# Kernel tuning notes

Measured on AMD Instinct MI355X. Metric: run time of the kernel, lower is better.

The kernel has to match this reference:

```python
import jax, jax.numpy as jnp
import numpy as np

N = 100000
E = 1600000
IN_CH = 128
HID = 16
HEADS = 4
OUT_CH = 2
EDGE_DIM = 3
NEG_SLOPE = 0.2


def gat_layer(x, src, dst, e_feat, W, att_src, att_dst, We, att_edge, bias, H, C, concat):
    # x: [N, Fin] -> projected [N, H, C]
    xs = (x @ W).reshape(-1, H, C)
    a_src = jnp.sum(xs * att_src, axis=-1)          # [N, H]
    a_dst = jnp.sum(xs * att_dst, axis=-1)          # [N, H]
    ee = (e_feat @ We).reshape(-1, H, C)            # [E, H, C]
    a_edge = jnp.sum(ee * att_edge, axis=-1)        # [E, H]
    alpha = a_src[src] + a_dst[dst] + a_edge        # [E, H]
    alpha = jax.nn.leaky_relu(alpha, NEG_SLOPE)
    # segment softmax over incoming edges of each dst node
    seg_max = jax.ops.segment_max(alpha, dst, num_segments=N)
    alpha = jnp.exp(alpha - seg_max[dst])
    seg_sum = jax.ops.segment_sum(alpha, dst, num_segments=N)
    alpha = alpha / (seg_sum[dst] + 1e-16)
    # weighted message aggregation
    msg = xs[src] * alpha[:, :, None]               # [E, H, C]
    out = jax.ops.segment_sum(msg, dst, num_segments=N)  # [N, H, C]
    out = out.reshape(-1, H * C) if concat else out.mean(axis=1)
    return out + bias


def setup_inputs() -> dict:
    key = jax.random.key(0)
    ks = jax.random.split(key, 24)
    g = lambda i, shape, scale=0.1: jax.random.normal(ks[i], shape, dtype=jnp.float32) * scale
    inp = {
        "x": jax.random.normal(ks[0], (N, IN_CH), dtype=jnp.float32),
        "edge_index": jax.random.randint(ks[1], (2, E), 0, N, dtype=jnp.int32),
        "edge_feat": jax.random.normal(ks[2], (E, EDGE_DIM), dtype=jnp.float32),
        # edge MLP
        "Em1": g(3, (EDGE_DIM, EDGE_DIM)), "eb1": g(4, (EDGE_DIM,)),
        "Em2": g(5, (EDGE_DIM, EDGE_DIM)), "eb2": g(6, (EDGE_DIM,)),
        # conv1: in -> HID per head, HEADS heads, concat
        "W1": g(7, (IN_CH, HEADS * HID)),
        "as1": g(8, (HEADS, HID)), "ad1": g(9, (HEADS, HID)),
        "We1": g(10, (EDGE_DIM, HEADS * HID)), "ae1": g(11, (HEADS, HID)),
        "b1": g(12, (HEADS * HID,)),
        # conv2: HEADS*HID -> OUT_CH, 1 head, no concat
        "W2": g(13, (HEADS * HID, OUT_CH)),
        "as2": g(14, (1, OUT_CH)), "ad2": g(15, (1, OUT_CH)),
        "We2": g(16, (EDGE_DIM, OUT_CH)), "ae2": g(17, (1, OUT_CH)),
        "b2": g(18, (OUT_CH,)),
    }
    return inp


def reference(x, edge_index, edge_feat,
              Em1, eb1, Em2, eb2,
              W1, as1, ad1, We1, ae1, b1,
              W2, as2, ad2, We2, ae2, b2):
    src, dst = edge_index[0], edge_index[1]
    # edge MLP: Linear -> ReLU -> Linear
    e = jax.nn.relu(edge_feat @ Em1 + eb1) @ Em2 + eb2
    # dropout layers are identity in eval mode
    h = gat_layer(x, src, dst, e, W1, as1, ad1, We1, ae1, b1, HEADS, HID, concat=True)
    h = jax.nn.elu(h)
    out = gat_layer(h, src, dst, e, W2, as2, ad2, We2, ae2, b2, 1, OUT_CH, concat=False)
    return out
```

## Files before the change

### kernel.cpp

```cpp
#include <hip/hip_runtime.h>
#include <hip/hip_fp16.h>
#include <math.h>
#include <stdint.h>

#define NEG_SLOPE 0.2f
#define SCAN_TILE 2048

__device__ __forceinline__ float leaky(float a) { return a > 0.f ? a : NEG_SLOPE * a; }
__device__ __forceinline__ __half2 u2h2(unsigned u) { return *reinterpret_cast<__half2*>(&u); }

__global__ __launch_bounds__(256) void k_pw(const int* __restrict__ dst, int* __restrict__ deg8,
                                            int* __restrict__ pw, int E, int N,
                                            const float* __restrict__ We1, const float* __restrict__ ae1,
                                            const float* __restrict__ We2, const float* __restrict__ ae2,
                                            float* __restrict__ cw) {
    if (blockIdx.x == 0 && threadIdx.x == 0) {
        for (int i = 0; i < 3; i++)
            for (int h = 0; h < 4; h++) {
                float s = 0.f;
                for (int m = 0; m < 16; m++) s += We1[i*64 + h*16 + m] * ae1[h*16 + m];
                cw[i*4 + h] = s;
            }
        for (int i = 0; i < 3; i++) cw[12 + i] = We2[i*2]*ae2[0] + We2[i*2+1]*ae2[1];
    }
    int c = blockIdx.x & 7;
    int* deg = deg8 + (size_t)c * N;
    unsigned ctag = (unsigned)c << 28;
    int base = (blockIdx.x * blockDim.x + threadIdx.x) * 4;
    if (base >= E) return;
    if (base + 3 < E) {
        int4 dv = *reinterpret_cast<const int4*>(&dst[base]);
        int4 pv;
        pv.x = atomicAdd(&deg[dv.x], 1) | ctag;
        pv.y = atomicAdd(&deg[dv.y], 1) | ctag;
        pv.z = atomicAdd(&deg[dv.z], 1) | ctag;
        pv.w = atomicAdd(&deg[dv.w], 1) | ctag;
        *reinterpret_cast<int4*>(&pw[base]) = pv;
    } else {
        for (int i = base; i < E; i++) pw[i] = atomicAdd(&deg[dst[i]], 1) | ctag;
    }
}

__global__ __launch_bounds__(256) void k_scan_partial(const int* __restrict__ deg8, int* __restrict__ tsum, int N) {
    __shared__ int sh[256];
    int b = blockIdx.x, t = threadIdx.x;
    int base = b * SCAN_TILE + t * 8;
    int s = 0;
    if (base + 8 <= N) {
        for (int c = 0; c < 8; c++) {
            const int4* p4 = reinterpret_cast<const int4*>(deg8 + (size_t)c * N + base);
            int4 a = p4[0], bb = p4[1];
            s += a.x + a.y + a.z + a.w + bb.x + bb.y + bb.z + bb.w;
        }
    } else if (base < N) {
        for (int i = base; i < N; i++)
            for (int c = 0; c < 8; c++) s += deg8[(size_t)c * N + i];
    }
    sh[t] = s; __syncthreads();
    for (int o = 128; o > 0; o >>= 1) { if (t < o) sh[t] += sh[t + o]; __syncthreads(); }
    if (t == 0) tsum[b] = sh[0];
}

__global__ void k_scan_tsum(const int* __restrict__ tsum, int* __restrict__ toff,
                            int* __restrict__ rowptr, int nb, int N) {
    if (threadIdx.x == 0 && blockIdx.x == 0) {
        int run = 0;
        for (int i = 0; i < nb; i++) { toff[i] = run; run += tsum[i]; }
        rowptr[N] = run;
    }
}

__global__ __launch_bounds__(256) void k_scan_final(const int* __restrict__ deg8, const int* __restrict__ toff,
        int* __restrict__ rowptr, int* __restrict__ cmbi, int N) {
    __shared__ int sh[256];
    int b = blockIdx.x, t = threadIdx.x;
    int base = b * SCAN_TILE + t * 8;
    int vt[8]; int s = 0;
    #pragma unroll
    for (int i = 0; i < 8; i++) {
        int idx = base + i; int tot = 0;
        if (idx < N) {
            #pragma unroll
            for (int c = 0; c < 8; c++) tot += deg8[(size_t)c * N + idx];
        }
        vt[i] = tot; s += tot;
    }
    sh[t] = s; __syncthreads();
    for (int o = 1; o < 256; o <<= 1) {
        int u = (t >= o) ? sh[t - o] : 0;
        __syncthreads();
        sh[t] += u;
        __syncthreads();
    }
    int run = sh[t] - s + toff[b];
    #pragma unroll
    for (int i = 0; i < 8; i++) {
        int idx = base + i;
        if (idx < N) {
            rowptr[idx] = run;
            int off = run;
            #pragma unroll
            for (int c = 0; c < 8; c++) {
                cmbi[(size_t)idx * 16 + 4 + c] = off;
                off += deg8[(size_t)c * N + idx];
            }
            run += vt[i];
        }
    }
}

__global__ __launch_bounds__(256) void k_proj1(const float* __restrict__ x, const float* __restrict__ W1,
        const float* __restrict__ as1, const float* __restrict__ ad1,
        __half* __restrict__ xs1h, float* __restrict__ as1v, float* __restrict__ cmbf, int N) {
    __shared__ float xr[32][128];
    int tid = threadIdx.x;
    int wave = tid >> 6, lane = tid & 63;
    int nbase = blockIdx.x * 32;
    if (nbase + 32 <= N) {
        const float4* x4 = reinterpret_cast<const float4*>(x + (size_t)nbase * 128);
        #pragma unroll
        for (int i = 0; i < 4; i++) {
            int idx = tid + i * 256;
            reinterpret_cast<float4*>(&xr[0][0])[idx] = x4[idx];
        }
    } else {
        for (int i = 0; i < 16; i++) {
            int flat = tid + i * 256;
            int row = flat >> 7, col = flat & 127;
            int n = nbase + row; if (n >= N) n = N - 1;
            xr[row][col] = x[(size_t)n * 128 + col];
        }
    }
    __syncthreads();
    int cc = lane & 15, kk = lane >> 4;
    int nw = wave * 8;
    const float4* W4 = reinterpret_cast<const float4*>(W1);
    float4 acc[8];
    #pragma unroll
    for (int m = 0; m < 8; m++) acc[m] = make_float4(0.f, 0.f, 0.f, 0.f);
    #pragma unroll 4
    for (int k = kk; k < 128; k += 4) {
        float4 wv = W4[k * 16 + cc];
        #pragma unroll
        for (int m = 0; m < 8; m++) {
            float xv = xr[nw + m][k];
            acc[m].x = fmaf(xv, wv.x, acc[m].x);
            acc[m].y = fmaf(xv, wv.y, acc[m].y);
            acc[m].z = fmaf(xv, wv.z, acc[m].z);
            acc[m].w = fmaf(xv, wv.w, acc[m].w);
        }
    }
    float a_s0 = as1[4*cc], a_s1 = as1[4*cc+1], a_s2 = as1[4*cc+2], a_s3 = as1[4*cc+3];
    float a_d0 = ad1[4*cc], a_d1 = ad1[4*cc+1], a_d2 = ad1[4*cc+2], a_d3 = ad1[4*cc+3];
    #pragma unroll
    for (int m = 0; m < 8; m++) {
        float4 a = acc[m];
        a.x += __shfl_xor(a.x, 16, 64); a.y += __shfl_xor(a.y, 16, 64);
        a.z += __shfl_xor(a.z, 16, 64); a.w += __shfl_xor(a.w, 16, 64);
        a.x += __shfl_xor(a.x, 32, 64); a.y += __shfl_xor(a.y, 32, 64);
        a.z += __shfl_xor(a.z, 32, 64); a.w += __shfl_xor(a.w, 32, 64);
        float ps = a.x*a_s0 + a.y*a_s1 + a.z*a_s2 + a.w*a_s3;
        float pd = a.x*a_d0 + a.y*a_d1 + a.z*a_d2 + a.w*a_d3;
        ps += __shfl_xor(ps, 1, 64); ps += __shfl_xor(ps, 2, 64);
        pd += __shfl_xor(pd, 1, 64); pd += __shfl_xor(pd, 2, 64);
        if (kk == 0) {
            int n = nbase + nw + m; if (n >= N) n = N - 1;
            __half2 h01 = __halves2half2(__float2half_rn(a.x), __float2half_rn(a.y));
            __half2 h23 = __halves2half2(__float2half_rn(a.z), __float2half_rn(a.w));
            uint2 st;
            st.x = *reinterpret_cast<unsigned*>(&h01);
            st.y = *reinterpret_cast<unsigned*>(&h23);
            *reinterpret_cast<uint2*>(&xs1h[(size_t)n*64 + 4*cc]) = st;
            if ((cc & 3) == 0) {
                int h = cc >> 2;
                as1v[n*4 + h] = ps;
                cmbf[(size_t)n*16 + h] = pd;
            }
        }
    }
}

__global__ __launch_bounds__(256) void k_payload(const float* __restrict__ ef,
                       const float* __restrict__ Em1, const float* __restrict__ eb1,
                       const float* __restrict__ Em2, const float* __restrict__ eb2,
                       const float* __restrict__ cw,
                       const int* __restrict__ src, const int* __restrict__ dst,
                       const int* __restrict__ pw,
                       const float4* __restrict__ as1v4,
                       const float* __restrict__ cmbf, const int* __restrict__ cmbi,
                       uint4* __restrict__ csr_pk, int E) {
    int base = (blockIdx.x * blockDim.x + threadIdx.x) * 4;
    if (base >= E) return;
    int cnt = min(4, E - base);

    float f[4][3]; int sv[4], dv[4], pv[4];
    if (cnt == 4) {
        const float4* ef4 = reinterpret_cast<const float4*>(ef);
        float4 a = ef4[base*3/4 + 0], b = ef4[base*3/4 + 1], c = ef4[base*3/4 + 2];
        f[0][0]=a.x; f[0][1]=a.y; f[0][2]=a.z;
        f[1][0]=a.w; f[1][1]=b.x; f[1][2]=b.y;
        f[2][0]=b.z; f[2][1]=b.w; f[2][2]=c.x;
        f[3][0]=c.y; f[3][1]=c.z; f[3][2]=c.w;
        int4 s4 = *reinterpret_cast<const int4*>(&src[base]);
        int4 d4 = *reinterpret_cast<const int4*>(&dst[base]);
        int4 p4 = *reinterpret_cast<const int4*>(&pw[base]);
        sv[0]=s4.x; sv[1]=s4.y; sv[2]=s4.z; sv[3]=s4.w;
        dv[0]=d4.x; dv[1]=d4.y; dv[2]=d4.z; dv[3]=d4.w;
        pv[0]=p4.x; pv[1]=p4.y; pv[2]=p4.z; pv[3]=p4.w;
    } else {
        for (int i = 0; i < cnt; i++) {
            f[i][0]=ef[(base+i)*3+0]; f[i][1]=ef[(base+i)*3+1]; f[i][2]=ef[(base+i)*3+2];
            sv[i]=src[base+i]; dv[i]=dst[base+i]; pv[i]=pw[base+i];
        }
    }

    #pragma unroll
    for (int i = 0; i < 4; i++) {
        if (i >= cnt) break;
        float f0=f[i][0], f1=f[i][1], f2=f[i][2];
        float t0 = fmaxf(f0*Em1[0]+f1*Em1[3]+f2*Em1[6]+eb1[0], 0.f);
        float t1 = fmaxf(f0*Em1[1]+f1*Em1[4]+f2*Em1[7]+eb1[1], 0.f);
        float t2 = fmaxf(f0*Em1[2]+f1*Em1[5]+f2*Em1[8]+eb1[2], 0.f);
        float u0 = t0*Em2[0]+t1*Em2[3]+t2*Em2[6]+eb2[0];
        float u1 = t0*Em2[1]+t1*Em2[4]+t2*Em2[7]+eb2[1];
        float u2 = t0*Em2[2]+t1*Em2[5]+t2*Em2[8]+eb2[2];
        int s = sv[i], d = dv[i];
        float4 av = as1v4[s];
        float4 bv = *reinterpret_cast<const float4*>(&cmbf[(size_t)d*16]);
        int c  = ((unsigned)pv[i]) >> 28;
        int ps = pv[i] & 0x0FFFFFFF;
        int slot = cmbi[(size_t)d*16 + 4 + c] + ps;
        float w0 = __expf(leaky(av.x + bv.x + u0*cw[0] + u1*cw[4] + u2*cw[8]));
        float w1 = __expf(leaky(av.y + bv.y + u0*cw[1] + u1*cw[5] + u2*cw[9]));
        float w2 = __expf(leaky(av.z + bv.z + u0*cw[2] + u1*cw[6] + u2*cw[10]));
        float w3 = __expf(leaky(av.w + bv.w + u0*cw[3] + u1*cw[7] + u2*cw[11]));
        float e2 = u0*cw[12] + u1*cw[13] + u2*cw[14];
        __half2 lo = __halves2half2(__float2half_rn(w0), __float2half_rn(w1));
        __half2 hi = __halves2half2(__float2half_rn(w2), __float2half_rn(w3));
        uint4 pki;
        pki.x = (unsigned)s;
        pki.y = *reinterpret_cast<unsigned*>(&lo);
        pki.z = *reinterpret_cast<unsigned*>(&hi);
        pki.w = *reinterpret_cast<unsigned*>(&e2);
        csr_pk[slot] = pki;
    }
}

__global__ __launch_bounds__(256, 4) void k_gat1(
        const int* __restrict__ rowptr, const uint4* __restrict__ csr_pk,
        const __half* __restrict__ xs1h,
        const float* __restrict__ b1, const float* __restrict__ W2,
        const float* __restrict__ as2, const float* __restrict__ ad2,
        float2* __restrict__ pk2, float* __restrict__ ad2v, int N) {
    int wave = threadIdx.x >> 6, lane = threadIdx.x & 63;
    int d = blockIdx.x * 4 + wave;
    if (d >= N) return;
    int beg = rowptr[d], end = rowptr[d+1];
    int cg = lane & 15, e4 = lane >> 4;
    int hh = cg >> 2;
    const __half* xbase = xs1h + 4 * cg;
    float4 acc = make_float4(0.f, 0.f, 0.f, 0.f);
    float4 wv  = make_float4(0.f, 0.f, 0.f, 0.f);
    for (int off = beg; off < end; off += 16) {
        int j = off + cg;
        uint4 p = make_uint4(0u, 0u, 0u, 0u);
        if (j < end) p = csr_pk[j];
        int si = (int)p.x;
        __half2 wl = u2h2(p.y), whp = u2h2(p.z);
        wv.x += __low2float(wl);  wv.y += __high2float(wl);
        wv.z += __low2float(whp); wv.w += __high2float(whp);
        int st0, st1, st2, st3; float wt0, wt1, wt2, wt3;
        {
            int sl0 = 0*4 + e4, sl1 = 1*4 + e4, sl2 = 2*4 + e4, sl3 = 3*4 + e4;
            st0 = __shfl(si, sl0, 16); st1 = __shfl(si, sl1, 16);
            st2 = __shfl(si, sl2, 16); st3 = __shfl(si, sl3, 16);
            unsigned y0 = __shfl(p.y, sl0, 16), z0 = __shfl(p.z, sl0, 16);
            unsigned y1 = __shfl(p.y, sl1, 16), z1 = __shfl(p.z, sl1, 16);
            unsigned y2 = __shfl(p.y, sl2, 16), z2 = __shfl(p.z, sl2, 16);
            unsigned y3 = __shfl(p.y, sl3, 16), z3 = __shfl(p.z, sl3, 16);
            unsigned q0 = (hh < 2) ? y0 : z0;
            unsigned q1 = (hh < 2) ? y1 : z1;
            unsigned q2 = (hh < 2) ? y2 : z2;
            unsigned q3 = (hh < 2) ? y3 : z3;
            wt0 = (hh & 1) ? __high2float(u2h2(q0)) : __low2float(u2h2(q0));
            wt1 = (hh & 1) ? __high2float(u2h2(q1)) : __low2float(u2h2(q1));
            wt2 = (hh & 1) ? __high2float(u2h2(q2)) : __low2float(u2h2(q2));
            wt3 = (hh & 1) ? __high2float(u2h2(q3)) : __low2float(u2h2(q3));
        }
        uint2 g0 = *reinterpret_cast<const uint2*>(xbase + ((size_t)st0 << 6));
        uint2 g1 = *reinterpret_cast<const uint2*>(xbase + ((size_t)st1 << 6));
        uint2 g2 = *reinterpret_cast<const uint2*>(xbase + ((size_t)st2 << 6));
        uint2 g3 = *reinterpret_cast<const uint2*>(xbase + ((size_t)st3 << 6));
        __half2 a, b;
        a = u2h2(g0.x); b = u2h2(g0.y);
        acc.x = fmaf(wt0, __low2float(a), acc.x); acc.y = fmaf(wt0, __high2float(a), acc.y);
        acc.z = fmaf(wt0, __low2float(b), acc.z); acc.w = fmaf(wt0, __high2float(b), acc.w);
        a = u2h2(g1.x); b = u2h2(g1.y);
        acc.x = fmaf(wt1, __low2float(a), acc.x); acc.y = fmaf(wt1, __high2float(a), acc.y);
        acc.z = fmaf(wt1, __low2float(b), acc.z); acc.w = fmaf(wt1, __high2float(b), acc.w);
        a = u2h2(g2.x); b = u2h2(g2.y);
        acc.x = fmaf(wt2, __low2float(a), acc.x); acc.y = fmaf(wt2, __high2float(a), acc.y);
        acc.z = fmaf(wt2, __low2float(b), acc.z); acc.w = fmaf(wt2, __high2float(b), acc.w);
        a = u2h2(g3.x); b = u2h2(g3.y);
        acc.x = fmaf(wt3, __low2float(a), acc.x); acc.y = fmaf(wt3, __high2float(a), acc.y);
        acc.z = fmaf(wt3, __low2float(b), acc.z); acc.w = fmaf(wt3, __high2float(b), acc.w);
    }
    acc.x += __shfl_xor(acc.x, 16, 64); acc.y += __shfl_xor(acc.y, 16, 64);
    acc.z += __shfl_xor(acc.z, 16, 64); acc.w += __shfl_xor(acc.w, 16, 64);
    acc.x += __shfl_xor(acc.x, 32, 64); acc.y += __shfl_xor(acc.y, 32, 64);
    acc.z += __shfl_xor(acc.z, 32, 64); acc.w += __shfl_xor(acc.w, 32, 64);
    #pragma unroll
    for (int o = 1; o <= 8; o <<= 1) {
        wv.x += __shfl_xor(wv.x, o, 16); wv.y += __shfl_xor(wv.y, o, 16);
        wv.z += __shfl_xor(wv.z, o, 16); wv.w += __shfl_xor(wv.w, o, 16);
    }
    float sm = (hh == 0) ? wv.x : (hh == 1) ? wv.y : (hh == 2) ? wv.z : wv.w;
    float inv = 1.f / (sm + 1e-16f);
    float v0 = acc.x * inv + b1[4*cg + 0];
    float v1 = acc.y * inv + b1[4*cg + 1];
    float v2 = acc.z * inv + b1[4*cg + 2];
    float v3 = acc.w * inv + b1[4*cg + 3];
    v0 = v0 > 0.f ? v0 : expm1f(v0);
    v1 = v1 > 0.f ? v1 : expm1f(v1);
    v2 = v2 > 0.f ? v2 : expm1f(v2);
    v3 = v3 > 0.f ? v3 : expm1f(v3);
    float p0 = v0*W2[(4*cg+0)*2] + v1*W2[(4*cg+1)*2] + v2*W2[(4*cg+2)*2] + v3*W2[(4*cg+3)*2];
    float p1 = v0*W2[(4*cg+0)*2+1] + v1*W2[(4*cg+1)*2+1] + v2*W2[(4*cg+2)*2+1] + v3*W2[(4*cg+3)*2+1];
    #pragma unroll
    for (int o = 1; o <= 8; o <<= 1) { p0 += __shfl_xor(p0, o, 16); p1 += __shfl_xor(p1, o, 16); }
    if (lane == 0) {
        float2 q;
        q.x = p0*as2[0] + p1*as2[1];
        __half2 xv = __halves2half2(__float2half_rn(p0), __float2half_rn(p1));
        q.y = *reinterpret_cast<float*>(&xv);
        pk2[d] = q;
        ad2v[d] = p0*ad2[0] + p1*ad2[1];
    }
}

__global__ __launch_bounds__(256) void k_gat2(
        const int* __restrict__ rowptr, const uint4* __restrict__ csr_pk,
        const float2* __restrict__ pk2, const float* __restrict__ ad2v,
        const float* __restrict__ b2, float* __restrict__ out, int N) {
    int t = blockIdx.x * blockDim.x + threadIdx.x;
    int d = t >> 4, j16 = t & 15;
    if (d >= N) return;
    int beg = rowptr[d], end = rowptr[d+1];
    float add = ad2v[d];
    float sm = 0.f, p0 = 0.f, p1 = 0.f;
    for (int off = beg; off < end; off += 16) {
        int j = off + j16;
        if (j < end) {
            uint4 p = csr_pk[j];
            int s = (int)p.x;
            float ea2 = *reinterpret_cast<float*>(&p.w);
            float2 q = pk2[s];
            float w = __expf(leaky(q.x + add + ea2));
            __half2 xv = *reinterpret_cast<__half2*>(&q.y);
            p0 = fmaf(w, __low2float(xv), p0);
            p1 = fmaf(w, __high2float(xv), p1);
            sm += w;
        }
    }
    #pragma unroll
    for (int o = 1; o < 16; o <<= 1) {
        sm += __shfl_xor(sm, o, 16);
        p0 += __shfl_xor(p0, o, 16);
        p1 += __shfl_xor(p1, o, 16);
    }
    if (j16 == 0) {
        float inv = 1.f / (sm + 1e-16f);
        out[d*2+0] = p0*inv + b2[0];
        out[d*2+1] = p1*inv + b2[1];
    }
}

extern "C" void kernel_launch(void* const* d_in, const int* in_sizes, int n_in,
                              void* d_out, int out_size, void* d_ws, size_t ws_size,
                              hipStream_t stream) {
    const float* x   = (const float*)d_in[0];
    const int*   ei  = (const int*)d_in[1];
    const float* ef  = (const float*)d_in[2];
    const float* Em1 = (const float*)d_in[3];
    const float* eb1 = (const float*)d_in[4];
    const float* Em2 = (const float*)d_in[5];
    const float* eb2 = (const float*)d_in[6];
    const float* W1  = (const float*)d_in[7];
    const float* as1 = (const float*)d_in[8];
    const float* ad1 = (const float*)d_in[9];
    const float* We1 = (const float*)d_in[10];
    const float* ae1 = (const float*)d_in[11];
    const float* b1  = (const float*)d_in[12];
    const float* W2  = (const float*)d_in[13];
    const float* as2 = (const float*)d_in[14];
    const float* ad2 = (const float*)d_in[15];
    const float* We2 = (const float*)d_in[16];
    const float* ae2 = (const float*)d_in[17];
    const float* b2  = (const float*)d_in[18];

    const int N = in_sizes[0] / 128;
    const int E = in_sizes[1] / 2;
    const int* srcp = ei;
    const int* dstp = ei + E;

    uintptr_t w = (uintptr_t)d_ws;
    auto alloc = [&](size_t bytes) -> void* {
        uintptr_t p = w; w += (bytes + 255) & ~(size_t)255; return (void*)p;
    };
    const int nb = (N + SCAN_TILE - 1) / SCAN_TILE;
    int*    deg8    = (int*)alloc((size_t)8 * N * sizeof(int));
    int*    rowptr  = (int*)alloc(((size_t)N + 1) * sizeof(int));
    int*    tsum    = (int*)alloc((size_t)nb * sizeof(int));
    int*    toff    = (int*)alloc((size_t)(nb + 1) * sizeof(int));
    float*  cw      = (float*)alloc(16 * sizeof(float));
    int*    pw      = (int*)alloc((size_t)E * sizeof(int));
    uint4*  csr_pk  = (uint4*)alloc((size_t)E * sizeof(uint4));
    __half* xs1h    = (__half*)alloc((size_t)N * 64 * sizeof(__half));
    float*  as1v    = (float*)alloc((size_t)N * 4 * sizeof(float));
    float*  cmb     = (float*)alloc((size_t)N * 16 * sizeof(float));
    float2* pk2     = (float2*)alloc((size_t)N * sizeof(float2));
    float*  ad2v    = (float*)alloc((size_t)N * sizeof(float));

    const int B = 256;

    hipMemsetAsync(deg8, 0, (size_t)8 * N * sizeof(int), stream);
    k_pw<<<(E/4+B-1)/B + 1, B, 0, stream>>>(dstp, deg8, pw, E, N, We1, ae1, We2, ae2, cw);
    k_scan_partial<<<nb, 256, 0, stream>>>(deg8, tsum, N);
    k_scan_tsum<<<1, 64, 0, stream>>>(tsum, toff, rowptr, nb, N);
    k_scan_final<<<nb, 256, 0, stream>>>(deg8, toff, rowptr, (int*)cmb, N);
    k_proj1<<<(N+31)/32, 256, 0, stream>>>(x, W1, as1, ad1, xs1h, as1v, cmb, N);
    k_payload<<<(E/4+B-1)/B + 1, B, 0, stream>>>(ef, Em1, eb1, Em2, eb2, cw,
                                                 srcp, dstp, pw, (const float4*)as1v,
                                                 cmb, (const int*)cmb, csr_pk, E);
    k_gat1<<<(N+3)/4, 256, 0, stream>>>(rowptr, csr_pk, xs1h, b1, W2, as2, ad2, pk2, ad2v, N);
    k_gat2<<<(N*16+B-1)/B, B, 0, stream>>>(rowptr, csr_pk, pk2, ad2v, b2, (float*)d_out, N);
}
```

Before: 269.2 us.

## Move dst-side attention and exp into gat1; pack slot offsets into 16-byte record

The scatter kernel no longer gathers the 64-byte per-destination record holding the a_dst scores and eight per-chunk offsets. It now reads a compact 16-byte record with the row start plus 8-bit packed chunk prefixes, and stores only the pre-activation source+edge logit in half precision. The dst logit add, leaky ReLU and exp are deferred to k_gat1, which loads a_dst once per destination node. This cuts random-gather traffic in the payload pass, at the cost of extra exp work in gat1 and the assumption that chunk prefixes fit in 8 bits (degree under 256). Storing logits instead of weights in fp16 also changes rounding.

```diff
diff --git a/kernel.cpp b/kernel.cpp
--- a/kernel.cpp
+++ b/kernel.cpp
@@ -71,7 +71,7 @@
 }
 
 __global__ __launch_bounds__(256) void k_scan_final(const int* __restrict__ deg8, const int* __restrict__ toff,
-        int* __restrict__ rowptr, int* __restrict__ cmbi, int N) {
+        int* __restrict__ rowptr, uint4* __restrict__ slotrec, int N) {
     __shared__ int sh[256];
     int b = blockIdx.x, t = threadIdx.x;
     int base = b * SCAN_TILE + t * 8;
@@ -98,12 +98,14 @@
         int idx = base + i;
         if (idx < N) {
             rowptr[idx] = run;
-            int off = run;
+            unsigned lo = 0, hi = 0; int off = 0;
             #pragma unroll
             for (int c = 0; c < 8; c++) {
-                cmbi[(size_t)idx * 16 + 4 + c] = off;
+                unsigned v = (unsigned)off & 0xFFu;
+                if (c < 4) lo |= v << (8*c); else hi |= v << (8*(c-4));
                 off += deg8[(size_t)c * N + idx];
             }
+            slotrec[idx] = make_uint4((unsigned)run, lo, hi, 0u);
             run += vt[i];
         }
     }
@@ -111,7 +113,7 @@
 
 __global__ __launch_bounds__(256) void k_proj1(const float* __restrict__ x, const float* __restrict__ W1,
         const float* __restrict__ as1, const float* __restrict__ ad1,
-        __half* __restrict__ xs1h, float* __restrict__ as1v, float* __restrict__ cmbf, int N) {
+        __half* __restrict__ xs1h, float* __restrict__ as1v, float* __restrict__ ad1v, int N) {
     __shared__ float xr[32][128];
     int tid = threadIdx.x;
     int wave = tid >> 6, lane = tid & 63;
@@ -174,7 +176,7 @@
             if ((cc & 3) == 0) {
                 int h = cc >> 2;
                 as1v[n*4 + h] = ps;
-                cmbf[(size_t)n*16 + h] = pd;
+                ad1v[n*4 + h] = pd;
             }
         }
     }
@@ -187,7 +189,7 @@
                        const int* __restrict__ src, const int* __restrict__ dst,
                        const int* __restrict__ pw,
                        const float4* __restrict__ as1v4,
-                       const float* __restrict__ cmbf, const int* __restrict__ cmbi,
+                       const uint4* __restrict__ slotrec,
                        uint4* __restrict__ csr_pk, int E) {
     int base = (blockIdx.x * blockDim.x + threadIdx.x) * 4;
     if (base >= E) return;
@@ -226,17 +228,18 @@
         float u2 = t0*Em2[2]+t1*Em2[5]+t2*Em2[8]+eb2[2];
         int s = sv[i], d = dv[i];
         float4 av = as1v4[s];
-        float4 bv = *reinterpret_cast<const float4*>(&cmbf[(size_t)d*16]);
+        uint4  r  = slotrec[d];
         int c  = ((unsigned)pv[i]) >> 28;
         int ps = pv[i] & 0x0FFFFFFF;
-        int slot = cmbi[(size_t)d*16 + 4 + c] + ps;
-        float w0 = __expf(leaky(av.x + bv.x + u0*cw[0] + u1*cw[4] + u2*cw[8]));
-        float w1 = __expf(leaky(av.y + bv.y + u0*cw[1] + u1*cw[5] + u2*cw[9]));
-        float w2 = __expf(leaky(av.z + bv.z + u0*cw[2] + u1*cw[6] + u2*cw[10]));
-        float w3 = __expf(leaky(av.w + bv.w + u0*cw[3] + u1*cw[7] + u2*cw[11]));
+        unsigned pre = ((c < 4) ? (r.y >> (8*c)) : (r.z >> (8*(c-4)))) & 0xFFu;
+        int slot = (int)r.x + (int)pre + ps;
+        float b0 = av.x + u0*cw[0] + u1*cw[4] + u2*cw[8];
+        float b1 = av.y + u0*cw[1] + u1*cw[5] + u2*cw[9];
+        float b2 = av.z + u0*cw[2] + u1*cw[6] + u2*cw[10];
+        float b3 = av.w + u0*cw[3] + u1*cw[7] + u2*cw[11];
         float e2 = u0*cw[12] + u1*cw[13] + u2*cw[14];
-        __half2 lo = __halves2half2(__float2half_rn(w0), __float2half_rn(w1));
-        __half2 hi = __halves2half2(__float2half_rn(w2), __float2half_rn(w3));
+        __half2 lo = __halves2half2(__float2half_rn(b0), __float2half_rn(b1));
+        __half2 hi = __halves2half2(__float2half_rn(b2), __float2half_rn(b3));
         uint4 pki;
         pki.x = (unsigned)s;
         pki.y = *reinterpret_cast<unsigned*>(&lo);
@@ -248,7 +251,7 @@
 
 __global__ __launch_bounds__(256, 4) void k_gat1(
         const int* __restrict__ rowptr, const uint4* __restrict__ csr_pk,
-        const __half* __restrict__ xs1h,
+        const __half* __restrict__ xs1h, const float4* __restrict__ ad1v4,
         const float* __restrict__ b1, const float* __restrict__ W2,
         const float* __restrict__ as2, const float* __restrict__ ad2,
         float2* __restrict__ pk2, float* __restrict__ ad2v, int N) {
@@ -256,6 +259,7 @@
     int d = blockIdx.x * 4 + wave;
     if (d >= N) return;
     int beg = rowptr[d], end = rowptr[d+1];
+    float4 ad4 = ad1v4[d];
     int cg = lane & 15, e4 = lane >> 4;
     int hh = cg >> 2;
     const __half* xbase = xs1h + 4 * cg;
@@ -263,21 +267,31 @@
     float4 wv  = make_float4(0.f, 0.f, 0.f, 0.f);
     for (int off = beg; off < end; off += 16) {
         int j = off + cg;
-        uint4 p = make_uint4(0u, 0u, 0u, 0u);
-        if (j < end) p = csr_pk[j];
+        bool valid = j < end;
+        uint4 p = valid ? csr_pk[j] : make_uint4(0u, 0u, 0u, 0u);
         int si = (int)p.x;
-        __half2 wl = u2h2(p.y), whp = u2h2(p.z);
-        wv.x += __low2float(wl);  wv.y += __high2float(wl);
-        wv.z += __low2float(whp); wv.w += __high2float(whp);
+        float w0 = 0.f, w1 = 0.f, w2 = 0.f, w3 = 0.f;
+        if (valid) {
+            __half2 l01 = u2h2(p.y), l23 = u2h2(p.z);
+            w0 = __expf(leaky(__low2float(l01)  + ad4.x));
+            w1 = __expf(leaky(__high2float(l01) + ad4.y));
+            w2 = __expf(leaky(__low2float(l23)  + ad4.z));
+            w3 = __expf(leaky(__high2float(l23) + ad4.w));
+        }
+        wv.x += w0; wv.y += w1; wv.z += w2; wv.w += w3;
+        __half2 wy2 = __halves2half2(__float2half_rn(w0), __float2half_rn(w1));
+        __half2 wz2 = __halves2half2(__float2half_rn(w2), __float2half_rn(w3));
+        unsigned wy = *reinterpret_cast<unsigned*>(&wy2);
+        unsigned wz = *reinterpret_cast<unsigned*>(&wz2);
         int st0, st1, st2, st3; float wt0, wt1, wt2, wt3;
         {
             int sl0 = 0*4 + e4, sl1 = 1*4 + e4, sl2 = 2*4 + e4, sl3 = 3*4 + e4;
             st0 = __shfl(si, sl0, 16); st1 = __shfl(si, sl1, 16);
             st2 = __shfl(si, sl2, 16); st3 = __shfl(si, sl3, 16);
-            unsigned y0 = __shfl(p.y, sl0, 16), z0 = __shfl(p.z, sl0, 16);
-            unsigned y1 = __shfl(p.y, sl1, 16), z1 = __shfl(p.z, sl1, 16);
-            unsigned y2 = __shfl(p.y, sl2, 16), z2 = __shfl(p.z, sl2, 16);
-            unsigned y3 = __shfl(p.y, sl3, 16), z3 = __shfl(p.z, sl3, 16);
+            unsigned y0 = __shfl(wy, sl0, 16), z0 = __shfl(wz, sl0, 16);
+            unsigned y1 = __shfl(wy, sl1, 16), z1 = __shfl(wz, sl1, 16);
+            unsigned y2 = __shfl(wy, sl2, 16), z2 = __shfl(wz, sl2, 16);
+            unsigned y3 = __shfl(wy, sl3, 16), z3 = __shfl(wz, sl3, 16);
             unsigned q0 = (hh < 2) ? y0 : z0;
             unsigned q1 = (hh < 2) ? y1 : z1;
             unsigned q2 = (hh < 2) ? y2 : z2;
@@ -414,10 +428,11 @@
     int*    toff    = (int*)alloc((size_t)(nb + 1) * sizeof(int));
     float*  cw      = (float*)alloc(16 * sizeof(float));
     int*    pw      = (int*)alloc((size_t)E * sizeof(int));
+    uint4*  slotrec = (uint4*)alloc((size_t)N * sizeof(uint4));
     uint4*  csr_pk  = (uint4*)alloc((size_t)E * sizeof(uint4));
     __half* xs1h    = (__half*)alloc((size_t)N * 64 * sizeof(__half));
     float*  as1v    = (float*)alloc((size_t)N * 4 * sizeof(float));
-    float*  cmb     = (float*)alloc((size_t)N * 16 * sizeof(float));
+    float*  ad1v    = (float*)alloc((size_t)N * 4 * sizeof(float));
     float2* pk2     = (float2*)alloc((size_t)N * sizeof(float2));
     float*  ad2v    = (float*)alloc((size_t)N * sizeof(float));
 
@@ -427,11 +442,12 @@
     k_pw<<<(E/4+B-1)/B + 1, B, 0, stream>>>(dstp, deg8, pw, E, N, We1, ae1, We2, ae2, cw);
     k_scan_partial<<<nb, 256, 0, stream>>>(deg8, tsum, N);
     k_scan_tsum<<<1, 64, 0, stream>>>(tsum, toff, rowptr, nb, N);
-    k_scan_final<<<nb, 256, 0, stream>>>(deg8, toff, rowptr, (int*)cmb, N);
-    k_proj1<<<(N+31)/32, 256, 0, stream>>>(x, W1, as1, ad1, xs1h, as1v, cmb, N);
+    k_scan_final<<<nb, 256, 0, stream>>>(deg8, toff, rowptr, slotrec, N);
+    k_proj1<<<(N+31)/32, 256, 0, stream>>>(x, W1, as1, ad1, xs1h, as1v, ad1v, N);
     k_payload<<<(E/4+B-1)/B + 1, B, 0, stream>>>(ef, Em1, eb1, Em2, eb2, cw,
                                                  srcp, dstp, pw, (const float4*)as1v,
-                                                 cmb, (const int*)cmb, csr_pk, E);
-    k_gat1<<<(N+3)/4, 256, 0, stream>>>(rowptr, csr_pk, xs1h, b1, W2, as2, ad2, pk2, ad2v, N);
+                                                 slotrec, csr_pk, E);
+    k_gat1<<<(N+3)/4, 256, 0, stream>>>(rowptr, csr_pk, xs1h, (const float4*)ad1v,
+                                        b1, W2, as2, ad2, pk2, ad2v, N);
     k_gat2<<<(N*16+B-1)/B, B, 0, stream>>>(rowptr, csr_pk, pk2, ad2v, b2, (float*)d_out, N);
 }
```

New measurement: 254.1 us. -5.6%, faster.
